# Kernel optimization log

Measured on AMD Instinct MI355X. Metric: run time of the kernel, lower is better.

The kernel has to match this reference:

```python
import jax, jax.numpy as jnp
import numpy as np

N_NODES = 10000
N_EDGES = 320000
IN_DIM = 64
HIDDEN = 128
HEADS = 4
OUT_DIM = 64
NEG_SLOPE = 0.2  # PyG GATConv default leaky_relu slope


def setup_inputs() -> dict:
    key = jax.random.key(0)
    ks = jax.random.split(key, 20)
    s = 0.05
    inp = {
        "x": jax.random.normal(ks[0], (N_NODES, IN_DIM), jnp.float32),
        "edge_index": jax.random.randint(ks[1], (2, N_EDGES), 0, N_NODES, jnp.int64),
        # GRU layer 0 (input IN_DIM -> HIDDEN), gates ordered [r, z, n] as in torch
        "w_ih0": jax.random.normal(ks[2], (3 * HIDDEN, IN_DIM), jnp.float32) * s,
        "w_hh0": jax.random.normal(ks[3], (3 * HIDDEN, HIDDEN), jnp.float32) * s,
        "b_ih0": jax.random.normal(ks[4], (3 * HIDDEN,), jnp.float32) * s,
        "b_hh0": jax.random.normal(ks[5], (3 * HIDDEN,), jnp.float32) * s,
        # GRU layer 1 (HIDDEN -> HIDDEN)
        "w_ih1": jax.random.normal(ks[6], (3 * HIDDEN, HIDDEN), jnp.float32) * s,
        "w_hh1": jax.random.normal(ks[7], (3 * HIDDEN, HIDDEN), jnp.float32) * s,
        "b_ih1": jax.random.normal(ks[8], (3 * HIDDEN,), jnp.float32) * s,
        "b_hh1": jax.random.normal(ks[9], (3 * HIDDEN,), jnp.float32) * s,
        # GAT layer 1: HIDDEN -> HIDDEN per head, HEADS heads, concat
        "W1": jax.random.normal(ks[10], (HIDDEN, HEADS * HIDDEN), jnp.float32) * s,
        "att_src1": jax.random.normal(ks[11], (HEADS, HIDDEN), jnp.float32) * s,
        "att_dst1": jax.random.normal(ks[12], (HEADS, HIDDEN), jnp.float32) * s,
        "bias1": jnp.zeros((HEADS * HIDDEN,), jnp.float32),
        # GAT layer 2: HEADS*HIDDEN -> OUT_DIM, 1 head
        "W2": jax.random.normal(ks[13], (HEADS * HIDDEN, OUT_DIM), jnp.float32) * s,
        "att_src2": jax.random.normal(ks[14], (1, OUT_DIM), jnp.float32) * s,
        "att_dst2": jax.random.normal(ks[15], (1, OUT_DIM), jnp.float32) * s,
        "bias2": jnp.zeros((OUT_DIM,), jnp.float32),
    }
    return inp


def _gru_layer(x, w_ih, w_hh, b_ih, b_hh):
    # x: [T, in]; torch GRU cell, unbatched, gates [r, z, n]
    H = w_hh.shape[1]
    gi = x @ w_ih.T + b_ih  # [T, 3H] precomputed input projections

    def step(h, gi_t):
        gh = h @ w_hh.T + b_hh
        i_r, i_z, i_n = jnp.split(gi_t, 3)
        h_r, h_z, h_n = jnp.split(gh, 3)
        r = jax.nn.sigmoid(i_r + h_r)
        z = jax.nn.sigmoid(i_z + h_z)
        n = jnp.tanh(i_n + r * h_n)
        h_new = (1.0 - z) * n + z * h
        return h_new, h_new

    h0 = jnp.zeros((H,), x.dtype)
    _, out = jax.lax.scan(step, h0, gi)
    return out  # [T, H]


def _gat(x, src, dst, W, att_src, att_dst, bias):
    # PyG GATConv (eval mode, add_self_loops=True, concat=True)
    N = x.shape[0]
    heads, C = att_src.shape
    h = (x @ W).reshape(N, heads, C)  # [N, H, C]
    loop = jnp.arange(N, dtype=src.dtype)
    s = jnp.concatenate([src, loop])
    d = jnp.concatenate([dst, loop])
    a_s = jnp.einsum("nhc,hc->nh", h, att_src)  # [N, H]
    a_d = jnp.einsum("nhc,hc->nh", h, att_dst)
    e = jax.nn.leaky_relu(a_s[s] + a_d[d], NEG_SLOPE)  # [E, H]
    m = jax.ops.segment_max(e, d, num_segments=N)  # per-dst max (every node has self loop)
    ex = jnp.exp(e - m[d])
    denom = jax.ops.segment_sum(ex, d, num_segments=N)
    alpha = ex / denom[d]  # [E, H]
    out = jax.ops.segment_sum(alpha[:, :, None] * h[s], d, num_segments=N)  # [N, H, C]
    return out.reshape(N, heads * C) + bias


def reference(x, edge_index,
              w_ih0, w_hh0, b_ih0, b_hh0,
              w_ih1, w_hh1, b_ih1, b_hh1,
              W1, att_src1, att_dst1, bias1,
              W2, att_src2, att_dst2, bias2):
    h = _gru_layer(x, w_ih0, w_hh0, b_ih0, b_hh0)
    h = _gru_layer(h, w_ih1, w_hh1, b_ih1, b_hh1)
    src, dst = edge_index[0], edge_index[1]
    h = _gat(h, src, dst, W1, att_src1, att_dst1, bias1)
    h = jax.nn.relu(h)
    out = _gat(h, src, dst, W2, att_src2, att_dst2, bias2)
    return out  # [N, OUT_DIM]
```

## Files before the change

kernel.cpp:

```cpp
#include <hip/hip_runtime.h>
#include <math.h>

#define NN_  10000
#define NE_  320000
#define IND  64
#define HID  128
#define G3   384
#define HC1  512
#define OUTD 64

typedef _Float16 h2f __attribute__((ext_vector_type(2)));
union UH4 { uint4 u; h2f h[4]; };

__device__ __forceinline__ float leakyf_(float x){ return x>0.f ? x : 0.2f*x; }
__device__ __forceinline__ float fsig_(float x){ return 1.f/(1.f+__expf(-x)); }
__device__ __forceinline__ float ftanh_(float x){ float e=__expf(2.f*x); return 1.f-2.f/(e+1.f); }

#define BARRIER_LDS() asm volatile("s_waitcnt lgkmcnt(0)\n\ts_barrier" ::: "memory")
#define WAIT_VM0()    asm volatile("s_waitcnt vmcnt(0)" ::: "memory")

__device__ __forceinline__ float ld_agent(const float* p) {
  return __hip_atomic_load(p, __ATOMIC_RELAXED, __HIP_MEMORY_SCOPE_AGENT);
}
__device__ __forceinline__ void st_agent(float* p, float v) {
  __hip_atomic_store(p, v, __ATOMIC_RELAXED, __HIP_MEMORY_SCOPE_AGENT);
}
__device__ __forceinline__ unsigned ld_agent_u32(const unsigned* p) {
  return __hip_atomic_load(p, __ATOMIC_RELAXED, __HIP_MEMORY_SCOPE_AGENT);
}
__device__ __forceinline__ void st_agent_u32(unsigned* p, unsigned v) {
  __hip_atomic_store(p, v, __ATOMIC_RELAXED, __HIP_MEMORY_SCOPE_AGENT);
}
__device__ __forceinline__ int ld_ctr(const int* p) {
  return __hip_atomic_load(p, __ATOMIC_ACQUIRE, __HIP_MEMORY_SCOPE_AGENT);
}
__device__ __forceinline__ void st_ctr(int* p, int v) {
  __hip_atomic_store(p, v, __ATOMIC_RELEASE, __HIP_MEMORY_SCOPE_AGENT);
}

template<bool TB>
__global__ __launch_bounds__(256) void gemm_k(const float* __restrict__ A,
                                              const float* __restrict__ B,
                                              const float* __restrict__ bias,
                                              float* __restrict__ C,
                                              int M, int N, int K) {
  __shared__ float As[16][65];
  __shared__ float Bs[16][65];
  const int bm = blockIdx.x * 64, bn = blockIdx.y * 64;
  const int tid = threadIdx.x;
  const int tm = (tid >> 4) << 2, tn = (tid & 15) << 2;
  float acc[4][4] = {};
  const int row = tid & 63, kq = (tid >> 6) << 2;
  for (int k0 = 0; k0 < K; k0 += 16) {
    float4 av = make_float4(0.f, 0.f, 0.f, 0.f);
    const int m = bm + row;
    if (m < M) av = *(const float4*)(A + (size_t)m * K + k0 + kq);
    As[kq + 0][row] = av.x; As[kq + 1][row] = av.y;
    As[kq + 2][row] = av.z; As[kq + 3][row] = av.w;
    if (TB) {
      float4 bv = *(const float4*)(B + (size_t)(bn + row) * K + k0 + kq);
      Bs[kq + 0][row] = bv.x; Bs[kq + 1][row] = bv.y;
      Bs[kq + 2][row] = bv.z; Bs[kq + 3][row] = bv.w;
    } else {
      const int kr = tid >> 4, nq = (tid & 15) << 2;
      float4 bv = *(const float4*)(B + (size_t)(k0 + kr) * N + bn + nq);
      Bs[kr][nq + 0] = bv.x; Bs[kr][nq + 1] = bv.y;
      Bs[kr][nq + 2] = bv.z; Bs[kr][nq + 3] = bv.w;
    }
    __syncthreads();
#pragma unroll
    for (int kk = 0; kk < 16; kk++) {
      float a[4], b[4];
#pragma unroll
      for (int i = 0; i < 4; i++) a[i] = As[kk][tm + i];
#pragma unroll
      for (int j = 0; j < 4; j++) b[j] = Bs[kk][tn + j];
#pragma unroll
      for (int i = 0; i < 4; i++)
#pragma unroll
        for (int j = 0; j < 4; j++) acc[i][j] = fmaf(a[i], b[j], acc[i][j]);
    }
    __syncthreads();
  }
#pragma unroll
  for (int i = 0; i < 4; i++) {
    const int m = bm + tm + i;
    if (m < M) {
#pragma unroll
      for (int j = 0; j < 4; j++) {
        const int n = bn + tn + j;
        float v = acc[i][j];
        if (bias) v += bias[n];
        C[(size_t)m * N + n] = v;
      }
    }
  }
}

__global__ __launch_bounds__(256, 1) void gru_pipe(const float* __restrict__ gi0,
                                                   const float* __restrict__ w_hh0,
                                                   const float* __restrict__ b_hh0,
                                                   const float* __restrict__ w_ih1,
                                                   const float* __restrict__ b_ih1,
                                                   const float* __restrict__ w_hh1,
                                                   const float* __restrict__ b_hh1,
                                                   unsigned* h0_st16, float* gi1_st,
                                                   int* ctr,
                                                   float* __restrict__ h1_out,
                                                   int T) {
  __shared__ _Float16 hbuf[2][HID];
  __shared__ float psum[3][HID];

  const int bid   = blockIdx.x;
  const int tid   = threadIdx.x;
  const int khalf = (tid >> 6) & 1;
  const int j     = (tid & 63) | ((tid >> 7) << 6);
  const int kbase = khalf * 64;

  const float* wsrc = (bid == 0) ? w_hh0 : (bid == 3 ? w_hh1 : w_ih1);
  const float* bsrc = (bid == 0) ? b_hh0 : (bid == 3 ? b_hh1 : b_ih1);

  h2f wr[32], wz[32], wn[32];
#pragma unroll
  for (int i = 0; i < 16; i++) {
    float4 a = *(const float4*)(wsrc + (size_t)j * HID + kbase + i * 4);
    wr[2 * i]     = h2f{(_Float16)a.x, (_Float16)a.y};
    wr[2 * i + 1] = h2f{(_Float16)a.z, (_Float16)a.w};
  }
#pragma unroll
  for (int i = 0; i < 16; i++) {
    float4 a = *(const float4*)(wsrc + (size_t)(j + HID) * HID + kbase + i * 4);
    wz[2 * i]     = h2f{(_Float16)a.x, (_Float16)a.y};
    wz[2 * i + 1] = h2f{(_Float16)a.z, (_Float16)a.w};
  }
#pragma unroll
  for (int i = 0; i < 16; i++) {
    float4 a = *(const float4*)(wsrc + (size_t)(j + 2 * HID) * HID + kbase + i * 4);
    wn[2 * i]     = h2f{(_Float16)a.x, (_Float16)a.y};
    wn[2 * i + 1] = h2f{(_Float16)a.z, (_Float16)a.w};
  }
  const float b0 = bsrc[j];
  const float b1 = bsrc[j + HID];
  const float b2 = bsrc[j + 2 * HID];

  auto dot_half = [&](const _Float16* hp16, float& r, float& z, float& n) {
    const uint4* hp = (const uint4*)(hp16 + kbase);
    float ar0 = 0.f, ar1 = 0.f, az0 = 0.f, az1 = 0.f, an0 = 0.f, an1 = 0.f;
#pragma unroll
    for (int c = 0; c < 2; c++) {
      uint4 hv[4];
#pragma unroll
      for (int i = 0; i < 4; i++) hv[i] = hp[c * 4 + i];
#pragma unroll
      for (int i = 0; i < 4; i++) {
        UH4 v; v.u = hv[i];
#pragma unroll
        for (int q = 0; q < 4; q++) {
          const int k = c * 16 + i * 4 + q;
          const h2f hh = v.h[q];
          if (k & 1) {
            ar1 = __builtin_amdgcn_fdot2(wr[k], hh, ar1, false);
            az1 = __builtin_amdgcn_fdot2(wz[k], hh, az1, false);
            an1 = __builtin_amdgcn_fdot2(wn[k], hh, an1, false);
          } else {
            ar0 = __builtin_amdgcn_fdot2(wr[k], hh, ar0, false);
            az0 = __builtin_amdgcn_fdot2(wz[k], hh, az0, false);
            an0 = __builtin_amdgcn_fdot2(wn[k], hh, an0, false);
          }
        }
      }
    }
    r = ar0 + ar1; z = az0 + az1; n = an0 + an1;
  };

  if (bid == 0 || bid == 3) {
    const float* gsrc = (bid == 0) ? gi0 : gi1_st;
    float hcur = 0.f;
    if (khalf == 0) hbuf[0][j] = (_Float16)0.f;
    BARRIER_LDS();

    if (bid == 3 && tid == 0) {
      while (ld_ctr(&ctr[1]) < 1) {}
      while (ld_ctr(&ctr[2]) < 2) {}
    }
    if (bid == 3) __syncthreads();

    float gxA, gyA, gzA, gxB, gyB, gzB;
    if (khalf == 0) {
      const float* gp = gsrc + j;
      gxA = gp[0]; gyA = gp[HID]; gzA = gp[2 * HID];
      gp = gsrc + G3 + j;
      gxB = gp[0]; gyB = gp[HID]; gzB = gp[2 * HID];
    }

    for (int t = 0; t < T; t += 2) {
      {
        float dr, dz, dn;
        dot_half(&hbuf[0][0], dr, dz, dn);
        if (khalf == 1) { psum[0][j] = dr; psum[1][j] = dz; psum[2][j] = dn; }
        BARRIER_LDS();
        if (khalf == 0) {
          const float r = fsig_(gxA + b0 + dr + psum[0][j]);
          const float z = fsig_(gyA + b1 + dz + psum[1][j]);
          const float n = ftanh_(gzA + r * (b2 + dn + psum[2][j]));
          hcur = (1.f - z) * n + z * hcur;
          hbuf[1][j] = (_Float16)hcur;
          if (bid == 3) h1_out[(size_t)t * HID + j] = hcur;
          const int tp = (t + 2 < T) ? (t + 2) : 0;
          const float* gp = gsrc + (size_t)tp * G3 + j;
          gxA = gp[0]; gyA = gp[HID]; gzA = gp[2 * HID];
        }
        if (bid == 3 && tid == 0 && (t & 15) == 0) {
          int need = t + 19; if (need > T) need = T;
          while (ld_ctr(&ctr[1]) < need) {}
          while (ld_ctr(&ctr[2]) < need) {}
        }
        BARRIER_LDS();
        if (bid == 0 && tid >= 64 && tid < 128) {
          const int idx = tid - 64;
          unsigned v = *(const unsigned*)&hbuf[1][2 * idx];
          st_agent_u32(&h0_st16[(size_t)t * 64 + idx], v);
        }
      }
      {
        const int tc = t + 1;
        float dr, dz, dn;
        dot_half(&hbuf[1][0], dr, dz, dn);
        if (khalf == 1) { psum[0][j] = dr; psum[1][j] = dz; psum[2][j] = dn; }
        BARRIER_LDS();
        if (khalf == 0) {
          const float r = fsig_(gxB + b0 + dr + psum[0][j]);
          const float z = fsig_(gyB + b1 + dz + psum[1][j]);
          const float n = ftanh_(gzB + r * (b2 + dn + psum[2][j]));
          hcur = (1.f - z) * n + z * hcur;
          hbuf[0][j] = (_Float16)hcur;
          if (bid == 3) h1_out[(size_t)tc * HID + j] = hcur;
          const int tp = (tc + 2 < T) ? (tc + 2) : 0;
          const float* gp = gsrc + (size_t)tp * G3 + j;
          gxB = gp[0]; gyB = gp[HID]; gzB = gp[2 * HID];
        }
        BARRIER_LDS();
        if (bid == 0 && tid >= 64 && tid < 128) {
          const int idx = tid - 64;
          unsigned v = *(const unsigned*)&hbuf[0][2 * idx];
          st_agent_u32(&h0_st16[(size_t)tc * 64 + idx], v);
          if ((tc & 3) == 3) {
            WAIT_VM0();
            if (tid == 64) st_ctr(&ctr[0], tc + 1);
          }
        }
      }
    }
    if (bid == 0 && tid >= 64 && tid < 128) {
      WAIT_VM0();
      if (tid == 64) st_ctr(&ctr[0], T);
    }
  } else {
    const int f = bid - 1;
    _Float16* hstage = &hbuf[0][0];
    int done = 0;
    for (int t = f; t < T; t += 2) {
      if (tid == 0) { while (ld_ctr(&ctr[0]) < t + 1) {} }
      __syncthreads();
      if (tid < 64)
        ((unsigned*)hstage)[tid] = ld_agent_u32(&h0_st16[(size_t)t * 64 + tid]);
      BARRIER_LDS();
      float dr, dz, dn;
      dot_half(hstage, dr, dz, dn);
      if (khalf == 1) { psum[0][j] = dr; psum[1][j] = dz; psum[2][j] = dn; }
      BARRIER_LDS();
      if (khalf == 0) {
        float* gp = gi1_st + (size_t)t * G3 + j;
        st_agent(gp,           dr + psum[0][j] + b0);
        st_agent(gp + HID,     dz + psum[1][j] + b1);
        st_agent(gp + 2 * HID, dn + psum[2][j] + b2);
      }
      done++;
      if ((done & 1) == 0) {
        __syncthreads();
        if (tid == 0) st_ctr(&ctr[1 + f], t + 1);
      }
    }
    __syncthreads();
    if (tid == 0) st_ctr(&ctr[1 + f], T);
  }
}

__global__ void att_dots(const float* __restrict__ feat,
                         const float* __restrict__ att_src,
                         const float* __restrict__ att_dst,
                         float* __restrict__ a_s, float* __restrict__ a_d,
                         int heads, int C) {
  const int n = blockIdx.x;
  const int h = threadIdx.x >> 6;
  const int lane = threadIdx.x & 63;
  float ss = 0.f, dd = 0.f;
  const float* f = feat + (size_t)n * heads * C + h * C;
  for (int c = lane; c < C; c += 64) {
    const float v = f[c];
    ss = fmaf(v, att_src[h * C + c], ss);
    dd = fmaf(v, att_dst[h * C + c], dd);
  }
#pragma unroll
  for (int o = 32; o > 0; o >>= 1) {
    ss += __shfl_down(ss, o);
    dd += __shfl_down(dd, o);
  }
  if (lane == 0) { a_s[n * heads + h] = ss; a_d[n * heads + h] = dd; }
}

__global__ void edge_count(const int* __restrict__ ei, int* __restrict__ cnt, int E) {
  const int e = blockIdx.x * 256 + threadIdx.x;
  if (e < E) atomicAdd(&cnt[ei[E + e]], 1);
}

__global__ __launch_bounds__(1024) void prefix_scan(const int* __restrict__ cnt,
                                                    int* __restrict__ offs,
                                                    int* __restrict__ cursor, int N) {
  __shared__ int buf[1024];
  __shared__ int carry;
  const int tid = threadIdx.x;
  if (tid == 0) carry = 0;
  __syncthreads();
  for (int base = 0; base < N; base += 1024) {
    const int i = base + tid;
    const int v = (i < N) ? cnt[i] : 0;
    buf[tid] = v;
    __syncthreads();
    for (int d = 1; d < 1024; d <<= 1) {
      int t = 0;
      if (tid >= d) t = buf[tid - d];
      __syncthreads();
      buf[tid] += t;
      __syncthreads();
    }
    const int incl = buf[tid] + carry;
    if (i < N) { offs[i] = incl - v; cursor[i] = incl - v; }
    __syncthreads();
    if (tid == 1023) carry = incl;
    __syncthreads();
  }
  if (tid == 0) offs[N] = carry;
}

__global__ void edge_fill(const int* __restrict__ ei, int* __restrict__ cursor,
                          int* __restrict__ csr, int E) {
  const int e = blockIdx.x * 256 + threadIdx.x;
  if (e < E) {
    const int d = ei[E + e];
    const int s = ei[e];
    const int pos = atomicAdd(&cursor[d], 1);
    csr[pos] = s;
  }
}

__global__ void gat_agg(const float* __restrict__ feat,
                        const float* __restrict__ a_s, const float* __restrict__ a_d,
                        const int* __restrict__ offs, const int* __restrict__ csr,
                        const float* __restrict__ bias, float* __restrict__ out,
                        int heads, int cshift, int do_relu) {
  const int n = blockIdx.x;
  const int t = threadIdx.x;
  const int HC = blockDim.x;
  const int h = t >> cshift;
  const int beg = offs[n], end = offs[n + 1];
  const float ad = a_d[n * heads + h];
  const float self_e = leakyf_(a_s[n * heads + h] + ad);
  float m = self_e;
  for (int i = beg; i < end; i++) {
    const int s = csr[i];
    m = fmaxf(m, leakyf_(a_s[s * heads + h] + ad));
  }
  float den = expf(self_e - m);
  float acc = den * feat[(size_t)n * HC + t];
  for (int i = beg; i < end; i++) {
    const int s = csr[i];
    const float wgt = expf(leakyf_(a_s[s * heads + h] + ad) - m);
    den += wgt;
    acc = fmaf(wgt, feat[(size_t)s * HC + t], acc);
  }
  float o = acc / den + bias[t];
  if (do_relu) o = fmaxf(o, 0.f);
  out[(size_t)n * HC + t] = o;
}

extern "C" void kernel_launch(void* const* d_in, const int* in_sizes, int n_in,
                              void* d_out, int out_size, void* d_ws, size_t ws_size,
                              hipStream_t stream) {
  const float* x        = (const float*)d_in[0];
  const int*   ei       = (const int*)d_in[1];
  const float* w_ih0    = (const float*)d_in[2];
  const float* w_hh0    = (const float*)d_in[3];
  const float* b_ih0    = (const float*)d_in[4];
  const float* b_hh0    = (const float*)d_in[5];
  const float* w_ih1    = (const float*)d_in[6];
  const float* w_hh1    = (const float*)d_in[7];
  const float* b_ih1    = (const float*)d_in[8];
  const float* b_hh1    = (const float*)d_in[9];
  const float* W1       = (const float*)d_in[10];
  const float* att_src1 = (const float*)d_in[11];
  const float* att_dst1 = (const float*)d_in[12];
  const float* bias1    = (const float*)d_in[13];
  const float* W2       = (const float*)d_in[14];
  const float* att_src2 = (const float*)d_in[15];
  const float* att_dst2 = (const float*)d_in[16];
  const float* bias2    = (const float*)d_in[17];
  float* out = (float*)d_out;

  const int N = NN_;
  const int E = in_sizes[1] / 2;

  float* f    = (float*)d_ws;
  float* gi   = f;
  float* hmm1 = f;
  float* h1   = f + (size_t)N * HC1;
  float* g1o  = h1 + (size_t)N * HID;
  float* hmm2 = g1o + (size_t)N * HC1;
  float* as1  = hmm2 + (size_t)N * OUTD;
  float* ad1  = as1 + (size_t)N * 4;
  float* as2  = ad1 + (size_t)N * 4;
  float* ad2  = as2 + (size_t)N;
  int* cnt    = (int*)(ad2 + (size_t)N);
  int* offs   = cnt + N;
  int* cursor = offs + (N + 1);
  int* csr    = cursor + N;
  int* ctr    = csr + E;
  unsigned* h0_st16 = (unsigned*)g1o;
  float*    gi1_st  = g1o + (size_t)N * 64;

  const int mblocks = (N + 63) / 64;

  gemm_k<true><<<dim3(mblocks, G3 / 64), 256, 0, stream>>>(x, w_ih0, b_ih0, gi, N, G3, IND);
  hipMemsetAsync(ctr, 0, 3 * sizeof(int), stream);
  gru_pipe<<<4, 256, 0, stream>>>(gi, w_hh0, b_hh0, w_ih1, b_ih1, w_hh1, b_hh1,
                                  h0_st16, gi1_st, ctr, h1, N);

  hipMemsetAsync(cnt, 0, (size_t)N * sizeof(int), stream);
  edge_count<<<(E + 255) / 256, 256, 0, stream>>>(ei, cnt, E);
  prefix_scan<<<1, 1024, 0, stream>>>(cnt, offs, cursor, N);
  edge_fill<<<(E + 255) / 256, 256, 0, stream>>>(ei, cursor, csr, E);

  gemm_k<false><<<dim3(mblocks, HC1 / 64), 256, 0, stream>>>(h1, W1, nullptr, hmm1, N, HC1, HID);
  att_dots<<<N, 4 * 64, 0, stream>>>(hmm1, att_src1, att_dst1, as1, ad1, 4, HID);
  gat_agg<<<N, HC1, 0, stream>>>(hmm1, as1, ad1, offs, csr, bias1, g1o, 4, 7, 1);

  gemm_k<false><<<dim3(mblocks, OUTD / 64), 256, 0, stream>>>(g1o, W2, nullptr, hmm2, N, OUTD, HC1);
  att_dots<<<N, 1 * 64, 0, stream>>>(hmm2, att_src2, att_dst2, as2, ad2, 1, OUTD);
  gat_agg<<<N, OUTD, 0, stream>>>(hmm2, as2, ad2, offs, csr, bias2, out, 1, 6, 0);
}
```

Baseline: 6.914 ms.

## Deepen GRU pipeline: 4-step unroll, batched counter publish and h0 loads

The recurrent GRU blocks now unroll four timesteps with gate inputs prefetched four steps ahead instead of two. The producer block publishes its progress counter every 8 steps instead of every 4. Consumer blocks wait for 8-step chunks, load four h0 vectors at once, and publish once per chunk. This cuts cross-block spin-wait and memory-latency overhead on the sequential critical path, at the cost of coarser synchronisation and a larger startup lag for the layer-1 block.

```diff
diff --git a/kernel.cpp b/kernel.cpp
--- a/kernel.cpp
+++ b/kernel.cpp
@@ -180,105 +180,106 @@
     BARRIER_LDS();
 
     if (bid == 3 && tid == 0) {
-      while (ld_ctr(&ctr[1]) < 1) {}
-      while (ld_ctr(&ctr[2]) < 2) {}
+      while (ld_ctr(&ctr[1]) < 4) {}
+      while (ld_ctr(&ctr[2]) < 4) {}
     }
     if (bid == 3) __syncthreads();
 
-    float gxA, gyA, gzA, gxB, gyB, gzB;
+    float gxA, gyA, gzA, gxB, gyB, gzB, gxC, gyC, gzC, gxD, gyD, gzD;
     if (khalf == 0) {
       const float* gp = gsrc + j;
       gxA = gp[0]; gyA = gp[HID]; gzA = gp[2 * HID];
-      gp = gsrc + G3 + j;
+      gp = gsrc + (size_t)1 * G3 + j;
       gxB = gp[0]; gyB = gp[HID]; gzB = gp[2 * HID];
-    }
-
-    for (int t = 0; t < T; t += 2) {
-      {
+      gp = gsrc + (size_t)2 * G3 + j;
+      gxC = gp[0]; gyC = gp[HID]; gzC = gp[2 * HID];
+      gp = gsrc + (size_t)3 * G3 + j;
+      gxD = gp[0]; gyD = gp[HID]; gzD = gp[2 * HID];
+    }
+
+    auto substep = [&](int tc, int pin, float& gx, float& gy, float& gz) {
+      float dr, dz, dn;
+      dot_half(&hbuf[pin][0], dr, dz, dn);
+      if (khalf == 1) { psum[0][j] = dr; psum[1][j] = dz; psum[2][j] = dn; }
+      BARRIER_LDS();
+      if (khalf == 0) {
+        const float r = fsig_(gx + b0 + dr + psum[0][j]);
+        const float z = fsig_(gy + b1 + dz + psum[1][j]);
+        const float n = ftanh_(gz + r * (b2 + dn + psum[2][j]));
+        hcur = (1.f - z) * n + z * hcur;
+        hbuf[pin ^ 1][j] = (_Float16)hcur;
+        if (bid == 3) h1_out[(size_t)tc * HID + j] = hcur;
+        const int tp = (tc + 4 < T) ? (tc + 4) : 0;
+        const float* gp = gsrc + (size_t)tp * G3 + j;
+        gx = gp[0]; gy = gp[HID]; gz = gp[2 * HID];
+      }
+      if (bid == 3 && tid == 0 && (tc & 31) == 0) {
+        int need = tc + 36; if (need > T) need = T;
+        while (ld_ctr(&ctr[1]) < need) {}
+        while (ld_ctr(&ctr[2]) < need) {}
+      }
+      BARRIER_LDS();
+      if (bid == 0 && tid >= 64 && tid < 128) {
+        const int idx = tid - 64;
+        unsigned v = *(const unsigned*)&hbuf[pin ^ 1][2 * idx];
+        st_agent_u32(&h0_st16[(size_t)tc * 64 + idx], v);
+        if ((tc & 7) == 7) {
+          WAIT_VM0();
+          if (tid == 64) st_ctr(&ctr[0], tc + 1);
+        }
+      }
+    };
+
+    for (int t = 0; t < T; t += 4) {
+      substep(t,     0, gxA, gyA, gzA);
+      substep(t + 1, 1, gxB, gyB, gzB);
+      substep(t + 2, 0, gxC, gyC, gzC);
+      substep(t + 3, 1, gxD, gyD, gzD);
+    }
+    if (bid == 0 && tid >= 64 && tid < 128) {
+      WAIT_VM0();
+      if (tid == 64) st_ctr(&ctr[0], T);
+    }
+  } else {
+    const int f = bid - 1;
+    _Float16* hstage = &hbuf[0][0];
+    for (int t0 = f; t0 < T; t0 += 8) {
+      if (tid == 0) {
+        int need = t0 + 7; if (need > T) need = T;
+        while (ld_ctr(&ctr[0]) < need) {}
+      }
+      __syncthreads();
+      unsigned hv0 = 0, hv1 = 0, hv2 = 0, hv3 = 0;
+      if (tid < 64) {
+        hv0 = ld_agent_u32(&h0_st16[(size_t)t0 * 64 + tid]);
+        if (t0 + 2 < T) hv1 = ld_agent_u32(&h0_st16[(size_t)(t0 + 2) * 64 + tid]);
+        if (t0 + 4 < T) hv2 = ld_agent_u32(&h0_st16[(size_t)(t0 + 4) * 64 + tid]);
+        if (t0 + 6 < T) hv3 = ld_agent_u32(&h0_st16[(size_t)(t0 + 6) * 64 + tid]);
+      }
+#pragma unroll
+      for (int k = 0; k < 4; k++) {
+        const int t = t0 + 2 * k;
+        if (t >= T) break;
+        if (tid < 64) {
+          const unsigned hv = (k == 0) ? hv0 : (k == 1) ? hv1 : (k == 2) ? hv2 : hv3;
+          ((unsigned*)hstage)[tid] = hv;
+        }
+        BARRIER_LDS();
         float dr, dz, dn;
-        dot_half(&hbuf[0][0], dr, dz, dn);
+        dot_half(hstage, dr, dz, dn);
         if (khalf == 1) { psum[0][j] = dr; psum[1][j] = dz; psum[2][j] = dn; }
         BARRIER_LDS();
         if (khalf == 0) {
-          const float r = fsig_(gxA + b0 + dr + psum[0][j]);
-          const float z = fsig_(gyA + b1 + dz + psum[1][j]);
-          const float n = ftanh_(gzA + r * (b2 + dn + psum[2][j]));
-          hcur = (1.f - z) * n + z * hcur;
-          hbuf[1][j] = (_Float16)hcur;
-          if (bid == 3) h1_out[(size_t)t * HID + j] = hcur;
-          const int tp = (t + 2 < T) ? (t + 2) : 0;
-          const float* gp = gsrc + (size_t)tp * G3 + j;
-          gxA = gp[0]; gyA = gp[HID]; gzA = gp[2 * HID];
+          float* gp = gi1_st + (size_t)t * G3 + j;
+          st_agent(gp,           dr + psum[0][j] + b0);
+          st_agent(gp + HID,     dz + psum[1][j] + b1);
+          st_agent(gp + 2 * HID, dn + psum[2][j] + b2);
         }
-        if (bid == 3 && tid == 0 && (t & 15) == 0) {
-          int need = t + 19; if (need > T) need = T;
-          while (ld_ctr(&ctr[1]) < need) {}
-          while (ld_ctr(&ctr[2]) < need) {}
-        }
-        BARRIER_LDS();
-        if (bid == 0 && tid >= 64 && tid < 128) {
-          const int idx = tid - 64;
-          unsigned v = *(const unsigned*)&hbuf[1][2 * idx];
-          st_agent_u32(&h0_st16[(size_t)t * 64 + idx], v);
-        }
-      }
-      {
-        const int tc = t + 1;
-        float dr, dz, dn;
-        dot_half(&hbuf[1][0], dr, dz, dn);
-        if (khalf == 1) { psum[0][j] = dr; psum[1][j] = dz; psum[2][j] = dn; }
-        BARRIER_LDS();
-        if (khalf == 0) {
-          const float r = fsig_(gxB + b0 + dr + psum[0][j]);
-          const float z = fsig_(gyB + b1 + dz + psum[1][j]);
-          const float n = ftanh_(gzB + r * (b2 + dn + psum[2][j]));
-          hcur = (1.f - z) * n + z * hcur;
-          hbuf[0][j] = (_Float16)hcur;
-          if (bid == 3) h1_out[(size_t)tc * HID + j] = hcur;
-          const int tp = (tc + 2 < T) ? (tc + 2) : 0;
-          const float* gp = gsrc + (size_t)tp * G3 + j;
-          gxB = gp[0]; gyB = gp[HID]; gzB = gp[2 * HID];
-        }
-        BARRIER_LDS();
-        if (bid == 0 && tid >= 64 && tid < 128) {
-          const int idx = tid - 64;
-          unsigned v = *(const unsigned*)&hbuf[0][2 * idx];
-          st_agent_u32(&h0_st16[(size_t)tc * 64 + idx], v);
-          if ((tc & 3) == 3) {
-            WAIT_VM0();
-            if (tid == 64) st_ctr(&ctr[0], tc + 1);
-          }
-        }
-      }
-    }
-    if (bid == 0 && tid >= 64 && tid < 128) {
-      WAIT_VM0();
-      if (tid == 64) st_ctr(&ctr[0], T);
-    }
-  } else {
-    const int f = bid - 1;
-    _Float16* hstage = &hbuf[0][0];
-    int done = 0;
-    for (int t = f; t < T; t += 2) {
-      if (tid == 0) { while (ld_ctr(&ctr[0]) < t + 1) {} }
+      }
       __syncthreads();
-      if (tid < 64)
-        ((unsigned*)hstage)[tid] = ld_agent_u32(&h0_st16[(size_t)t * 64 + tid]);
-      BARRIER_LDS();
-      float dr, dz, dn;
-      dot_half(hstage, dr, dz, dn);
-      if (khalf == 1) { psum[0][j] = dr; psum[1][j] = dz; psum[2][j] = dn; }
-      BARRIER_LDS();
-      if (khalf == 0) {
-        float* gp = gi1_st + (size_t)t * G3 + j;
-        st_agent(gp,           dr + psum[0][j] + b0);
-        st_agent(gp + HID,     dz + psum[1][j] + b1);
-        st_agent(gp + 2 * HID, dn + psum[2][j] + b2);
-      }
-      done++;
-      if ((done & 1) == 0) {
-        __syncthreads();
-        if (tid == 0) st_ctr(&ctr[1 + f], t + 1);
+      if (tid == 0) {
+        int pub = t0 + 8; if (pub > T) pub = T;
+        st_ctr(&ctr[1 + f], pub);
       }
     }
     __syncthreads();
```

Result: faster. 6.313 ms (-8.7%).
